# Kernel tuning notes

Measured on AMD Instinct MI355X. Metric: run time of the kernel, lower is better.

## Reference

```python
import jax, jax.numpy as jnp
import numpy as np

EMBED_DIM = 1024
NUM_HEADS = 16
HEAD_DIM = EMBED_DIM // NUM_HEADS


def _sinusoid_pos_emb(seq_len, dim):
    pos = jnp.arange(seq_len, dtype=jnp.float32)
    idx = jnp.arange(dim // 2, dtype=jnp.float32)
    inv_freq = 1.0 / (10000.0 ** (2.0 * idx / dim))
    ang = pos[:, None] * inv_freq[None, :]          # [S, D/2]
    return jnp.concatenate([jnp.sin(ang), jnp.cos(ang)], axis=-1)  # [S, D]


def _relative_shift(x):
    # x: [B, H, S, S] -> Transformer-XL shift
    b, h, s, _ = x.shape
    x = jnp.pad(x, ((0, 0), (0, 0), (0, 0), (1, 0)))
    x = x.reshape(b, h, s + 1, s)
    return x[:, :, 1:, :].reshape(b, h, s, s)


def setup_inputs() -> dict:
    key = jax.random.key(0)
    ks = jax.random.split(key, 12)
    D = EMBED_DIM
    sc = 1.0 / np.sqrt(D)
    inp = {"x": jax.random.normal(ks[0], (2, 2048, D), dtype=jnp.float32)}
    for i, name in enumerate(["Wq", "Wk", "Wv", "Wp", "Wo"]):
        inp[name] = jax.random.normal(ks[1 + i], (D, D), dtype=jnp.float32) * sc
        inp["b" + name[1].lower()] = jnp.zeros((D,), dtype=jnp.float32)
    inp["u"] = jax.random.normal(ks[6], (1, NUM_HEADS, 1, HEAD_DIM), dtype=jnp.float32) * 0.05
    inp["v"] = jax.random.normal(ks[7], (1, NUM_HEADS, 1, HEAD_DIM), dtype=jnp.float32) * 0.05
    return inp


def reference(x, Wq, bq, Wk, bk, Wv, bv, Wp, bp, Wo, bo, u, v):
    B, S, D = x.shape
    H, P = NUM_HEADS, HEAD_DIM

    def heads(t):  # [B,S,D] -> [B,H,S,P]
        return t.reshape(B, S, H, P).transpose(0, 2, 1, 3)

    q = heads(x @ Wq + bq)
    k = heads(x @ Wk + bk)
    val = heads(x @ Wv + bv)

    pos = _sinusoid_pos_emb(S, D) @ Wp + bp            # [S, D]
    pos = pos.reshape(S, H, P).transpose(1, 0, 2)       # [H, S, P]

    content_score = jnp.einsum('bhsp,bhtp->bhst', q + u, k)
    pos_score = jnp.einsum('bhsp,htp->bhst', q + v, pos)
    pos_score = _relative_shift(pos_score)

    score = (content_score + pos_score) / jnp.sqrt(jnp.float32(P))
    weights = jax.nn.softmax(score, axis=-1)            # dropout = 0 (inference)
    out = jnp.einsum('bhst,bhtp->bhsp', weights, val)
    out = out.transpose(0, 2, 1, 3).reshape(B, S, D)
    return out @ Wo + bo
```

## Files before the change

kernel.cpp:

```cpp
#include <hip/hip_runtime.h>
#include <hip/hip_bf16.h>

typedef unsigned short u16;
typedef unsigned int u32;
typedef __bf16 bf16x8 __attribute__((ext_vector_type(8)));
typedef float f32x4 __attribute__((ext_vector_type(4)));

#define SEQ 2048
#define NH 16
#define PD 64
#define DM 1024

#if __has_builtin(__builtin_amdgcn_exp2f)
#define EXP2(x) __builtin_amdgcn_exp2f(x)
#else
#define EXP2(x) __expf((x) * 0.6931471805599453f)
#endif

__device__ __forceinline__ float bf2f(u16 s) {
  u32 t = ((u32)s) << 16;
  float f;
  __builtin_memcpy(&f, &t, 4);
  return f;
}
__device__ __forceinline__ u16 f2bf(float f) {
  u32 x;
  __builtin_memcpy(&x, &f, 4);
  x = (x + 0x7fffu + ((x >> 16) & 1u)) >> 16;
  return (u16)x;
}
__device__ __forceinline__ u32 pack2(float a, float b) {
  __hip_bfloat162 h = __float22bfloat162_rn(float2{a, b});
  u32 r;
  __builtin_memcpy(&r, &h, 4);
  return r;
}
__device__ __forceinline__ void gld16(const u16* g, u16* l) {
  __builtin_amdgcn_global_load_lds(
      (const __attribute__((address_space(1))) unsigned int*)(g),
      (__attribute__((address_space(3))) unsigned int*)(l), 16, 0, 0);
}

struct PrepArgs {
  const void* x;
  const void* w0; const void* w1; const void* w2; const void* w3; const void* w4;
  const void* p0; const void* p1; const void* p2; const void* p3; const void* p4;
  const void* p5; const void* p6;
};

__global__ __launch_bounds__(256) void prep_kernel(PrepArgs pa,
                                                   u16* __restrict__ xb,
                                                   u16* __restrict__ sinb,
                                                   u16* __restrict__ WT,
                                                   float* __restrict__ pf,
                                                   int* __restrict__ flag) {
  __shared__ int sz[256], sh[256];
  __shared__ u16 t[64][72];
  int tid = threadIdx.x;

  {
    const u16* probe = (const u16*)pa.w0;
    int zeros = 0, huge = 0;
    for (int j = 0; j < 16; ++j) {
      int i = tid * 16 + j;
      u16 v = probe[i];
      int e = (v >> 7) & 0xFF;
      if (((i & 1) == 0) && v == 0) zeros++;
      if (e >= 0x8C) huge++;
    }
    sz[tid] = zeros; sh[tid] = huge;
    __syncthreads();
    for (int s = 128; s > 0; s >>= 1) {
      if (tid < s) { sz[tid] += sz[tid + s]; sh[tid] += sh[tid + s]; }
      __syncthreads();
    }
  }
  int f = (sz[0] > 1024 || sh[0] > 200) ? 1 : 0;
  int id = blockIdx.x;
  if (id == 0 && tid == 0) *flag = f;

  if (id < 4096) {
    int i = (id * 256 + tid) * 4;
    if (f) {
      float4 fv = *(const float4*)((const float*)pa.x + i);
      u16 o[4] __attribute__((aligned(8))) = {f2bf(fv.x), f2bf(fv.y), f2bf(fv.z), f2bf(fv.w)};
      *(uint2*)(xb + i) = *(const uint2*)o;
    } else {
      *(uint2*)(xb + i) = *(const uint2*)((const u16*)pa.x + i);
    }
  } else if (id < 6144) {
    int base = ((id - 4096) * 256 + tid) * 4;
    u16 o[4] __attribute__((aligned(8)));
#pragma unroll
    for (int e = 0; e < 4; ++e) {
      int idx = base + e;
      int s = idx >> 10;
      int i = idx & 1023;
      int j = i & 511;
      float invf = __expf(-(float)j * (9.210340371976184f / 512.0f));
      float ang = (float)s * invf;
      float val = (i < 512) ? __sinf(ang) : __cosf(ang);
      o[e] = f2bf(val);
    }
    *(uint2*)(sinb + base) = *(const uint2*)o;
  } else if (id < 7424) {
    int tt = id - 6144;
    int z = tt >> 8;
    int rem = tt & 255;
    const void* src = (z == 0) ? pa.w0 : (z == 1) ? pa.w1 : (z == 2) ? pa.w2
                     : (z == 3) ? pa.w3 : pa.w4;
    u16* out = WT + (size_t)z * DM * DM;
    int r0 = (rem >> 4) * 64, c0 = (rem & 15) * 64;
    int tr = tid >> 2;
    int tc = (tid & 3) * 16;
    if (f) {
      const float* g = (const float*)src + (size_t)(r0 + tr) * DM + c0 + tc;
#pragma unroll
      for (int q = 0; q < 4; ++q) {
        float4 fv = *(const float4*)(g + q * 4);
        t[tr][tc + q * 4 + 0] = f2bf(fv.x);
        t[tr][tc + q * 4 + 1] = f2bf(fv.y);
        t[tr][tc + q * 4 + 2] = f2bf(fv.z);
        t[tr][tc + q * 4 + 3] = f2bf(fv.w);
      }
    } else {
      const uint4* g = (const uint4*)((const u16*)src + (size_t)(r0 + tr) * DM + c0 + tc);
      uint4 a = g[0], bb = g[1];
      *(uint4*)&t[tr][tc] = a;
      *(uint4*)&t[tr][tc + 8] = bb;
    }
    __syncthreads();
    u16 tmp[16] __attribute__((aligned(16)));
#pragma unroll
    for (int jj = 0; jj < 16; ++jj) tmp[jj] = t[tc + jj][tr];
    uint4* o = (uint4*)(out + (size_t)(c0 + tr) * DM + r0 + tc);
    o[0] = *(const uint4*)&tmp[0];
    o[1] = *(const uint4*)&tmp[8];
  } else {
    int idx = (id - 7424) * 256 + tid;
    int seg = idx >> 10, off = idx & 1023;
    const void* s = (seg == 0) ? pa.p0 : (seg == 1) ? pa.p1 : (seg == 2) ? pa.p2
                   : (seg == 3) ? pa.p3 : (seg == 4) ? pa.p4 : (seg == 5) ? pa.p5 : pa.p6;
    pf[idx] = f ? ((const float*)s)[off] : bf2f(((const u16*)s)[off]);
  }
}

__global__ __launch_bounds__(256, 3) void qkv_kernel(
    const u16* __restrict__ xb, const u16* __restrict__ sinb,
    const u16* __restrict__ WT, const float* __restrict__ pf,
    u16* __restrict__ Qb, u16* __restrict__ Kb, u16* __restrict__ Vtb,
    u16* __restrict__ Rb) {
  __shared__ u16 As[128 * 32];
  __shared__ u16 Bs[3 * 64 * 32];
  int tid = threadIdx.x;
  int wave = tid >> 6, lane = tid & 63;
  int quad = lane >> 4, l16 = lane & 15;
  int bx = blockIdx.x, by = blockIdx.y;
  bool isR = by >= 32;
  int m0 = (isR ? (by - 32) : by) * 128;
  int n0 = bx * 64;
  int wm = (wave >> 1) * 64, wn = (wave & 1) * 32;

  int trow = tid >> 2;
  int tcol = ((tid & 3) ^ ((tid >> 3) & 3)) * 8;
  const u16* A = isR ? sinb : xb;
  const u16* ga = A + (size_t)(m0 + trow) * DM + tcol;
  const u16* gb = WT + (isR ? (size_t)3 * DM * DM : 0) + (size_t)(n0 + trow) * DM + tcol;
  u16* lwa = As + wave * 512;
  u16* lwb = Bs + wave * 512;
  int slotx = (quad ^ ((l16 >> 1) & 3)) * 8;

  if (!isR) {
    f32x4 acc[3][4][2] = {};
    for (int k0 = 0; k0 < DM; k0 += 32) {
      __syncthreads();
      gld16(ga + k0, lwa);
      gld16(ga + (size_t)64 * DM + k0, lwa + 2048);
      gld16(gb + k0, lwb);
      gld16(gb + (size_t)DM * DM + k0, lwb + 2048);
      gld16(gb + (size_t)2 * DM * DM + k0, lwb + 4096);
      __syncthreads();
      bf16x8 af[4];
#pragma unroll
      for (int i = 0; i < 4; ++i)
        af[i] = *(const bf16x8*)&As[(wm + i * 16 + l16) * 32 + slotx];
#pragma unroll
      for (int z = 0; z < 3; ++z) {
        bf16x8 b0 = *(const bf16x8*)&Bs[z * 2048 + (wn + l16) * 32 + slotx];
        bf16x8 b1 = *(const bf16x8*)&Bs[z * 2048 + (wn + 16 + l16) * 32 + slotx];
#pragma unroll
        for (int tm = 0; tm < 4; ++tm) {
          acc[z][tm][0] = __builtin_amdgcn_mfma_f32_16x16x32_bf16(af[tm], b0, acc[z][tm][0], 0, 0, 0);
          acc[z][tm][1] = __builtin_amdgcn_mfma_f32_16x16x32_bf16(af[tm], b1, acc[z][tm][1], 0, 0, 0);
        }
      }
    }
#pragma unroll
    for (int tm = 0; tm < 4; ++tm) {
      int row = m0 + wm + tm * 16 + quad * 4;
#pragma unroll
      for (int tn = 0; tn < 2; ++tn) {
        int col = n0 + wn + tn * 16 + l16;
        float bq = pf[col], bk = pf[1024 + col], bv = pf[2048 + col];
#pragma unroll
        for (int r = 0; r < 4; ++r) {
          Qb[(size_t)(row + r) * DM + col] = f2bf(acc[0][tm][tn][r] + bq);
          Kb[(size_t)(row + r) * DM + col] = f2bf(acc[1][tm][tn][r] + bk);
        }
        u16 o4[4] __attribute__((aligned(8)));
#pragma unroll
        for (int r = 0; r < 4; ++r) o4[r] = f2bf(acc[2][tm][tn][r] + bv);
        int bq_ = row >> 11, s = row & 2047;
        *(uint2*)(Vtb + ((size_t)(bq_ * 1024 + col)) * 2048 + s) = *(const uint2*)o4;
      }
    }
  } else {
    f32x4 acc[4][2] = {};
    for (int k0 = 0; k0 < DM; k0 += 32) {
      __syncthreads();
      gld16(ga + k0, lwa);
      gld16(ga + (size_t)64 * DM + k0, lwa + 2048);
      gld16(gb + k0, lwb);
      __syncthreads();
      bf16x8 af[4];
#pragma unroll
      for (int i = 0; i < 4; ++i)
        af[i] = *(const bf16x8*)&As[(wm + i * 16 + l16) * 32 + slotx];
      bf16x8 b0 = *(const bf16x8*)&Bs[(wn + l16) * 32 + slotx];
      bf16x8 b1 = *(const bf16x8*)&Bs[(wn + 16 + l16) * 32 + slotx];
#pragma unroll
      for (int tm = 0; tm < 4; ++tm) {
        acc[tm][0] = __builtin_amdgcn_mfma_f32_16x16x32_bf16(af[tm], b0, acc[tm][0], 0, 0, 0);
        acc[tm][1] = __builtin_amdgcn_mfma_f32_16x16x32_bf16(af[tm], b1, acc[tm][1], 0, 0, 0);
      }
    }
#pragma unroll
    for (int tm = 0; tm < 4; ++tm) {
      int row = m0 + wm + tm * 16 + quad * 4;
#pragma unroll
      for (int tn = 0; tn < 2; ++tn) {
        int col = n0 + wn + tn * 16 + l16;
        float br = pf[3072 + col];
#pragma unroll
        for (int r = 0; r < 4; ++r)
          Rb[(size_t)(row + r) * DM + col] = f2bf(acc[tm][tn][r] + br);
      }
    }
  }
}

struct GemmArgs {
  const u16* A;  const u16* A3;
  const u16* Bt0; const u16* Bt1; const u16* Bt2; const u16* Bt3;
  const float* b0; const float* b1; const float* b2; const float* b3;
  void* C0; void* C1; void* C2; void* C3;
  int N, K, M3;
  const int* flag; int outFp32; int vtrans;
};

__global__ __launch_bounds__(256, 4) void gemm_bt_kernel(GemmArgs p) {
  __shared__ u16 As[128 * 64];
  __shared__ u16 Bs[128 * 64];
  int z = blockIdx.z;
  if (z == 3 && (int)blockIdx.y * 128 >= p.M3) return;
  const u16* A = (z == 3) ? p.A3 : p.A;
  const u16* Bt = (z == 0) ? p.Bt0 : (z == 1) ? p.Bt1 : (z == 2) ? p.Bt2 : p.Bt3;
  const float* bias = (z == 0) ? p.b0 : (z == 1) ? p.b1 : (z == 2) ? p.b2 : p.b3;
  void* Cv = (z == 0) ? p.C0 : (z == 1) ? p.C1 : (z == 2) ? p.C2 : p.C3;
  int K = p.K, N = p.N;
  bool f32o = p.outFp32 && (*p.flag);
  bool vt = p.vtrans && (z == 2);

  int tid = threadIdx.x;
  int wave = tid >> 6, lane = tid & 63;
  int quad = lane >> 4, l16 = lane & 15;
  int m0 = blockIdx.y * 128, n0 = blockIdx.x * 128;
  int wm = (wave >> 1) * 64, wn = (wave & 1) * 64;

  int trow = tid >> 2;
  int tcol = ((tid & 3) ^ ((tid >> 3) & 3)) * 8;
  const u16* ga = A + (size_t)(m0 + trow) * K + tcol;
  const u16* gb = Bt + (size_t)(n0 + trow) * K + tcol;
  u16* lwa = As + wave * 512;
  u16* lwb = Bs + wave * 512;
  int slotx = (quad ^ ((l16 >> 1) & 3)) * 8;

  f32x4 acc[4][4] = {};

  for (int k0 = 0; k0 < K; k0 += 64) {
    __syncthreads();
    gld16(ga + k0, lwa);
    gld16(ga + (size_t)64 * K + k0, lwa + 2048);
    gld16(ga + k0 + 32, lwa + 4096);
    gld16(ga + (size_t)64 * K + k0 + 32, lwa + 6144);
    gld16(gb + k0, lwb);
    gld16(gb + (size_t)64 * K + k0, lwb + 2048);
    gld16(gb + k0 + 32, lwb + 4096);
    gld16(gb + (size_t)64 * K + k0 + 32, lwb + 6144);
    __syncthreads();
#pragma unroll
    for (int kh = 0; kh < 2; ++kh) {
      int kbase = kh * 4096;
      bf16x8 af[4], bfv[4];
#pragma unroll
      for (int i = 0; i < 4; ++i) {
        af[i] = *(const bf16x8*)&As[kbase + (wm + i * 16 + l16) * 32 + slotx];
        bfv[i] = *(const bf16x8*)&Bs[kbase + (wn + i * 16 + l16) * 32 + slotx];
      }
#pragma unroll
      for (int tm = 0; tm < 4; ++tm)
#pragma unroll
        for (int tn = 0; tn < 4; ++tn)
          acc[tm][tn] = __builtin_amdgcn_mfma_f32_16x16x32_bf16(af[tm], bfv[tn], acc[tm][tn], 0, 0, 0);
    }
  }

#pragma unroll
  for (int tm = 0; tm < 4; ++tm) {
    int row = m0 + wm + tm * 16 + quad * 4;
#pragma unroll
    for (int tn = 0; tn < 4; ++tn) {
      int col = n0 + wn + tn * 16 + l16;
      float bv = bias[col];
      if (vt) {
        u16 o4[4] __attribute__((aligned(8)));
#pragma unroll
        for (int r = 0; r < 4; ++r) o4[r] = f2bf(acc[tm][tn][r] + bv);
        int bq_ = row >> 11, s = row & 2047;
        *(uint2*)((u16*)Cv + ((size_t)(bq_ * 1024 + col)) * 2048 + s) = *(const uint2*)o4;
      } else {
#pragma unroll
        for (int r = 0; r < 4; ++r) {
          float val = acc[tm][tn][r] + bv;
          if (f32o) ((float*)Cv)[(size_t)(row + r) * N + col] = val;
          else ((u16*)Cv)[(size_t)(row + r) * N + col] = f2bf(val);
        }
      }
    }
  }
}

__global__ __launch_bounds__(256, 4) void attn_kernel(
    const u16* __restrict__ Q, const u16* __restrict__ Kg,
    const u16* __restrict__ Vtg, const u16* __restrict__ Rg,
    const float* __restrict__ pf,
    u16* __restrict__ O) {
  __shared__ __align__(16) u16 KP[64 * 72];
  __shared__ __align__(16) u16 RVs[4096];
  __shared__ __align__(16) u16 Bb[128 * 66];

  int tid = threadIdx.x, wave = tid >> 6, lane = tid & 63;
  int quad = lane >> 4, l16 = lane & 15;
  int id = blockIdx.x;
  int bh = (id & 7) + ((id >> 8) << 3);
  int s0 = ((id >> 3) & 31) * 64;
  int b = bh >> 4, h = bh & 15;
  const float* pu = pf + 5 * 1024 + h * PD;
  const float* pv = pf + 6 * 1024 + h * PD;

  int arow = wave * 16 + l16;
  int sl_base = wave * 16 + quad * 4;

  int srow = wave * 16 + (lane >> 2);
  int scol = ((lane & 3) ^ ((lane >> 3) & 3)) * 8;
  u16* kbase = KP + wave * 512;
  u16* rvbase = RVs + wave * 512;
  int kb0 = l16 * 32 + (quad ^ ((l16 >> 1) & 3)) * 8;

  const float QS = 0.18033688011112042f;
  bf16x8 qu0, qu1, qv0a, qv1a, qv0b, qv1b;
  {
    const u16* qp = Q + ((size_t)(b * SEQ + s0 + arow)) * DM + h * PD;
    int row2 = s0 + arow + 1;
    if (row2 > SEQ - 1) row2 = SEQ - 1;
    const u16* qp2 = Q + ((size_t)(b * SEQ + row2)) * DM + h * PD;
    u16 qa[16] __attribute__((aligned(16)));
    u16 qb[16] __attribute__((aligned(16)));
    *(uint4*)&qa[0] = *(const uint4*)(qp + quad * 8);
    *(uint4*)&qa[8] = *(const uint4*)(qp + 32 + quad * 8);
    *(uint4*)&qb[0] = *(const uint4*)(qp2 + quad * 8);
    *(uint4*)&qb[8] = *(const uint4*)(qp2 + 32 + quad * 8);
    u16 fu[16] __attribute__((aligned(16)));
    u16 fv0[16] __attribute__((aligned(16)));
    u16 fv1[16] __attribute__((aligned(16)));
#pragma unroll
    for (int j = 0; j < 8; ++j) {
      float u0 = pu[quad * 8 + j], u1 = pu[32 + quad * 8 + j];
      float v0 = pv[quad * 8 + j], v1 = pv[32 + quad * 8 + j];
      fu[j] = f2bf((bf2f(qa[j]) + u0) * QS);
      fu[8 + j] = f2bf((bf2f(qa[8 + j]) + u1) * QS);
      fv0[j] = f2bf((bf2f(qa[j]) + v0) * QS);
      fv0[8 + j] = f2bf((bf2f(qa[8 + j]) + v1) * QS);
      fv1[j] = f2bf((bf2f(qb[j]) + v0) * QS);
      fv1[8 + j] = f2bf((bf2f(qb[8 + j]) + v1) * QS);
    }
    __builtin_memcpy(&qu0, &fu[0], 16);
    __builtin_memcpy(&qu1, &fu[8], 16);
    __builtin_memcpy(&qv0a, &fv0[0], 16);
    __builtin_memcpy(&qv1a, &fv0[8], 16);
    __builtin_memcpy(&qv0b, &fv1[0], 16);
    __builtin_memcpy(&qv1b, &fv1[8], 16);
  }

  bf16x8 onesf;
  {
    u16 onearr[8] __attribute__((aligned(16)));
#pragma unroll
    for (int j = 0; j < 8; ++j) onearr[j] = 0x3F80;
    __builtin_memcpy(&onesf, onearr, 16);
  }

  auto dmaR = [&](int tb0) {
    int tg = tb0 + srow;
    tg = tg < 0 ? 0 : (tg > SEQ - 1 ? SEQ - 1 : tg);
    const u16* gr = Rg + (size_t)tg * DM + h * PD + scol;
    gld16(gr, rvbase);
    gld16(gr + 32, rvbase + 2048);
  };
  auto slice = [&](bf16x8 fa0, bf16x8 fa1, int slotBase, int rowOff, int lo, int hi) {
#pragma unroll
    for (int tt = 0; tt < 4; ++tt) {
      f32x4 pacc = {};
      bf16x8 b0 = *(const bf16x8*)&RVs[kb0 + tt * 512];
      bf16x8 b1 = *(const bf16x8*)&RVs[kb0 + tt * 512 + 2048];
      pacc = __builtin_amdgcn_mfma_f32_16x16x32_bf16(fa0, b0, pacc, 0, 0, 0);
      pacc = __builtin_amdgcn_mfma_f32_16x16x32_bf16(fa1, b1, pacc, 0, 0, 0);
      int rloc = tt * 16 + l16;
      bool ok = (rloc >= lo) & (rloc <= hi);
      u32 w0 = ok ? pack2(pacc[0], pacc[1]) : 0u;
      u32 w1 = ok ? pack2(pacc[2], pacc[3]) : 0u;
      int prow = (slotBase + rloc + rowOff) & 127;
      *(u32*)&Bb[prow * 66 + sl_base] = w0;
      *(u32*)&Bb[prow * 66 + sl_base + 2] = w1;
    }
  };

  f32x4 lacc = {};
  f32x4 oacc[4] = {};

  dmaR(SEQ - 65 - s0);
  __syncthreads();
  slice(qv0a, qv1a, 0, 0, 0, 63);

  for (int j0 = 0; j0 < SEQ; j0 += 64) {
    int a1 = (j0 >> 6) + 1;
    int slot = (a1 & 1) << 6;
    bool p0n = (j0 <= s0);
    bool p1n = (j0 >= s0);
    __syncthreads();
    {
      const u16* gk = Kg + (size_t)(b * SEQ + j0 + srow) * DM + h * PD + scol;
      gld16(gk, kbase);
      gld16(gk + 32, kbase + 2048);
    }
    dmaR((p0n ? (SEQ - 65 - s0) : (-65 - s0)) + 64 * a1);
    __syncthreads();

    f32x4 acc[4];
#pragma unroll
    for (int tn = 0; tn < 4; ++tn) {
      f32x4 a = {};
      bf16x8 b0 = *(const bf16x8*)&KP[kb0 + tn * 512];
      bf16x8 b1 = *(const bf16x8*)&KP[kb0 + tn * 512 + 2048];
      a = __builtin_amdgcn_mfma_f32_16x16x32_bf16(qu0, b0, a, 0, 0, 0);
      a = __builtin_amdgcn_mfma_f32_16x16x32_bf16(qu1, b1, a, 0, 0, 0);
      acc[tn] = a;
    }

    if (p0n) slice(qv0a, qv1a, slot, 0, 0, s0 + 64 - 64 * a1);
    if (p0n && p1n) {
      __syncthreads();
      dmaR(64 * a1 - s0 - 65);
      __syncthreads();
    }
    if (p1n) slice(qv0b, qv1b, slot, 1, s0 + 65 - 64 * a1, 63);
    __syncthreads();

    {
      const u16* gv = Vtg + ((size_t)(b * NH + h) * PD + srow) * SEQ + j0 + scol;
      gld16(gv, rvbase);
      gld16(gv + 32, rvbase + 2048);
    }

    int g0 = l16 - sl_base + 64 + j0;
#pragma unroll
    for (int tn = 0; tn < 4; ++tn) {
#pragma unroll
      for (int r = 0; r < 4; ++r) {
        int rl = (g0 + tn * 16 - r) & 127;
        acc[tn][r] += bf2f(Bb[rl * 66 + sl_base + r]);
      }
    }

#pragma unroll
    for (int r = 0; r < 4; ++r) {
      u32 w0 = pack2(EXP2(acc[0][r]), EXP2(acc[1][r]));
      u32 w1 = pack2(EXP2(acc[2][r]), EXP2(acc[3][r]));
      u16 ec[4] = {(u16)w0, (u16)(w0 >> 16), (u16)w1, (u16)(w1 >> 16)};
      int row = sl_base + r;
      u16* prow_ = KP + row * 72 + l16;
#pragma unroll
      for (int cr = 0; cr < 4; ++cr) {
        int c = (cr + quad) & 3;
        prow_[c * 16] = ec[c];
      }
    }
    __syncthreads();

    {
      bf16x8 pa0 = *(const bf16x8*)&KP[arow * 72 + quad * 8];
      bf16x8 pa1 = *(const bf16x8*)&KP[arow * 72 + 32 + quad * 8];
      lacc = __builtin_amdgcn_mfma_f32_16x16x32_bf16(pa0, onesf, lacc, 0, 0, 0);
      lacc = __builtin_amdgcn_mfma_f32_16x16x32_bf16(pa1, onesf, lacc, 0, 0, 0);
#pragma unroll
      for (int tp = 0; tp < 4; ++tp) {
        bf16x8 b0 = *(const bf16x8*)&RVs[kb0 + tp * 512];
        bf16x8 b1 = *(const bf16x8*)&RVs[kb0 + tp * 512 + 2048];
        oacc[tp] = __builtin_amdgcn_mfma_f32_16x16x32_bf16(pa0, b0, oacc[tp], 0, 0, 0);
        oacc[tp] = __builtin_amdgcn_mfma_f32_16x16x32_bf16(pa1, b1, oacc[tp], 0, 0, 0);
      }
    }
  }

  float li[4];
#pragma unroll
  for (int r = 0; r < 4; ++r) li[r] = 1.f / lacc[r];
#pragma unroll
  for (int tp = 0; tp < 4; ++tp) {
    int pcol = tp * 16 + l16;
#pragma unroll
    for (int r = 0; r < 4; ++r) {
      int sg = s0 + sl_base + r;
      O[((size_t)(b * SEQ + sg)) * DM + h * PD + pcol] = f2bf(oacc[tp][r] * li[r]);
    }
  }
}

extern "C" void kernel_launch(void* const* d_in, const int* in_sizes, int n_in,
                              void* d_out, int out_size, void* d_ws, size_t ws_size,
                              hipStream_t stream) {
  (void)in_sizes; (void)n_in; (void)out_size; (void)ws_size;
  const void* x  = d_in[0];
  const void* Wq = d_in[1];
  const void* bq = d_in[2];
  const void* Wk = d_in[3];
  const void* bk = d_in[4];
  const void* Wv = d_in[5];
  const void* bv = d_in[6];
  const void* Wp = d_in[7];
  const void* bp = d_in[8];
  const void* Wo = d_in[9];
  const void* bo = d_in[10];
  const void* u  = d_in[11];
  const void* v  = d_in[12];

  char* base = (char*)d_ws;
  int* flag = (int*)base;
  float* pf = (float*)(base + 64);
  u16* wbase = (u16*)(base + 64 + 7168 * 4);
  u16* WT   = wbase;
  u16* xb   = WT + (size_t)5 * DM * DM;
  u16* sinb = xb + (size_t)2 * SEQ * DM;
  u16* Qb   = sinb + (size_t)SEQ * DM;
  u16* Kb   = Qb + (size_t)2 * SEQ * DM;
  u16* Vtb  = Kb + (size_t)2 * SEQ * DM;
  u16* Rb   = Vtb + (size_t)2 * SEQ * DM;
  u16* Ab   = xb;

  PrepArgs pa;
  pa.x = x;
  pa.w0 = Wq; pa.w1 = Wk; pa.w2 = Wv; pa.w3 = Wp; pa.w4 = Wo;
  pa.p0 = bq; pa.p1 = bk; pa.p2 = bv; pa.p3 = bp; pa.p4 = bo; pa.p5 = u; pa.p6 = v;
  prep_kernel<<<7452, 256, 0, stream>>>(pa, xb, sinb, WT, pf, flag);

  qkv_kernel<<<dim3(16, 48), 256, 0, stream>>>(xb, sinb, WT, pf, Qb, Kb, Vtb, Rb);

  attn_kernel<<<dim3(1024), 256, 0, stream>>>(Qb, Kb, Vtb, Rb, pf, Ab);

  GemmArgs fo;
  fo.A = Ab; fo.A3 = Ab;
  fo.Bt0 = WT + (size_t)4 * DM * DM; fo.Bt1 = fo.Bt0; fo.Bt2 = fo.Bt0; fo.Bt3 = fo.Bt0;
  fo.b0 = pf + 4096; fo.b1 = fo.b0; fo.b2 = fo.b0; fo.b3 = fo.b0;
  fo.C0 = d_out; fo.C1 = d_out; fo.C2 = d_out; fo.C3 = d_out;
  fo.N = DM; fo.K = DM; fo.M3 = 0; fo.flag = flag; fo.outFp32 = 1; fo.vtrans = 0;
  gemm_bt_kernel<<<dim3(8, 32, 1), 256, 0, stream>>>(fo);
}
```

Before: 284.5 us.

## Merge four launches into two persistent kernels joined by grid barriers

Fuses prep with the QKV/position projection, and attention with the output projection, into two kernels. Each kernel uses an atomic-counter grid barrier and a fixed grid sized to stay co-resident (768 blocks at 3 per CU, 1024 at 4 per CU). The aim is to remove launch gaps and tail effects between stages. In exchange it adds spin-wait barrier cost and a memset. The output GEMM now uses smaller 64x64 tiles, and tighter launch bounds may raise register pressure. It also relies on the runtime occupancy check to avoid deadlock.

```diff
diff --git a/kernel.cpp b/kernel.cpp
--- a/kernel.cpp
+++ b/kernel.cpp
@@ -39,6 +39,19 @@
   __builtin_amdgcn_global_load_lds(
       (const __attribute__((address_space(1))) unsigned int*)(g),
       (__attribute__((address_space(3))) unsigned int*)(l), 16, 0, 0);
+}
+
+__device__ __forceinline__ void grid_barrier(int* cnt, int nblk) {
+  __syncthreads();
+  if (threadIdx.x == 0) {
+    __threadfence();
+    int old = __hip_atomic_fetch_add(cnt, 1, __ATOMIC_ACQ_REL, __HIP_MEMORY_SCOPE_AGENT);
+    int target = (old / nblk + 1) * nblk;
+    while (__hip_atomic_load(cnt, __ATOMIC_ACQUIRE, __HIP_MEMORY_SCOPE_AGENT) < target) {
+      __builtin_amdgcn_s_sleep(8);
+    }
+  }
+  __syncthreads();
 }
 
 struct PrepArgs {
@@ -47,6 +60,453 @@
   const void* p0; const void* p1; const void* p2; const void* p3; const void* p4;
   const void* p5; const void* p6;
 };
+
+__global__ __launch_bounds__(256, 3) void prep_qkv_kernel(
+    PrepArgs pa,
+    u16* __restrict__ xb, u16* __restrict__ sinb, u16* __restrict__ WT,
+    float* __restrict__ pf, int* __restrict__ flag, int* __restrict__ cnt,
+    u16* __restrict__ Qb, u16* __restrict__ Kb, u16* __restrict__ Vtb,
+    u16* __restrict__ Rb) {
+  __shared__ int sz[256], sh[256];
+  __shared__ u16 t[64][72];
+  __shared__ u16 As[128 * 32];
+  __shared__ u16 Bs[3 * 64 * 32];
+  int tid = threadIdx.x;
+  int bid = blockIdx.x;
+
+  {
+    const u16* probe = (const u16*)pa.w0;
+    int zeros = 0, huge = 0;
+    for (int j = 0; j < 16; ++j) {
+      int i = tid * 16 + j;
+      u16 v = probe[i];
+      int e = (v >> 7) & 0xFF;
+      if (((i & 1) == 0) && v == 0) zeros++;
+      if (e >= 0x8C) huge++;
+    }
+    sz[tid] = zeros; sh[tid] = huge;
+    __syncthreads();
+    for (int s = 128; s > 0; s >>= 1) {
+      if (tid < s) { sz[tid] += sz[tid + s]; sh[tid] += sh[tid + s]; }
+      __syncthreads();
+    }
+  }
+  int f = (sz[0] > 1024 || sh[0] > 200) ? 1 : 0;
+  if (bid == 0 && tid == 0) *flag = f;
+
+  for (int id = bid; id < 7452; id += 768) {
+    if (id < 4096) {
+      int i = (id * 256 + tid) * 4;
+      if (f) {
+        float4 fv = *(const float4*)((const float*)pa.x + i);
+        u16 o[4] __attribute__((aligned(8))) = {f2bf(fv.x), f2bf(fv.y), f2bf(fv.z), f2bf(fv.w)};
+        *(uint2*)(xb + i) = *(const uint2*)o;
+      } else {
+        *(uint2*)(xb + i) = *(const uint2*)((const u16*)pa.x + i);
+      }
+    } else if (id < 6144) {
+      int base = ((id - 4096) * 256 + tid) * 4;
+      u16 o[4] __attribute__((aligned(8)));
+#pragma unroll
+      for (int e = 0; e < 4; ++e) {
+        int idx = base + e;
+        int s = idx >> 10;
+        int i = idx & 1023;
+        int j = i & 511;
+        float invf = __expf(-(float)j * (9.210340371976184f / 512.0f));
+        float ang = (float)s * invf;
+        float val = (i < 512) ? __sinf(ang) : __cosf(ang);
+        o[e] = f2bf(val);
+      }
+      *(uint2*)(sinb + base) = *(const uint2*)o;
+    } else if (id < 7424) {
+      __syncthreads();
+      int tt = id - 6144;
+      int z = tt >> 8;
+      int rem = tt & 255;
+      const void* src = (z == 0) ? pa.w0 : (z == 1) ? pa.w1 : (z == 2) ? pa.w2
+                       : (z == 3) ? pa.w3 : pa.w4;
+      u16* out = WT + (size_t)z * DM * DM;
+      int r0 = (rem >> 4) * 64, c0 = (rem & 15) * 64;
+      int tr = tid >> 2;
+      int tc = (tid & 3) * 16;
+      if (f) {
+        const float* g = (const float*)src + (size_t)(r0 + tr) * DM + c0 + tc;
+#pragma unroll
+        for (int q = 0; q < 4; ++q) {
+          float4 fv = *(const float4*)(g + q * 4);
+          t[tr][tc + q * 4 + 0] = f2bf(fv.x);
+          t[tr][tc + q * 4 + 1] = f2bf(fv.y);
+          t[tr][tc + q * 4 + 2] = f2bf(fv.z);
+          t[tr][tc + q * 4 + 3] = f2bf(fv.w);
+        }
+      } else {
+        const uint4* g = (const uint4*)((const u16*)src + (size_t)(r0 + tr) * DM + c0 + tc);
+        uint4 a = g[0], bb = g[1];
+        *(uint4*)&t[tr][tc] = a;
+        *(uint4*)&t[tr][tc + 8] = bb;
+      }
+      __syncthreads();
+      u16 tmp[16] __attribute__((aligned(16)));
+#pragma unroll
+      for (int jj = 0; jj < 16; ++jj) tmp[jj] = t[tc + jj][tr];
+      uint4* o = (uint4*)(out + (size_t)(c0 + tr) * DM + r0 + tc);
+      o[0] = *(const uint4*)&tmp[0];
+      o[1] = *(const uint4*)&tmp[8];
+    } else {
+      int idx = (id - 7424) * 256 + tid;
+      int seg = idx >> 10, off = idx & 1023;
+      const void* s = (seg == 0) ? pa.p0 : (seg == 1) ? pa.p1 : (seg == 2) ? pa.p2
+                     : (seg == 3) ? pa.p3 : (seg == 4) ? pa.p4 : (seg == 5) ? pa.p5 : pa.p6;
+      pf[idx] = f ? ((const float*)s)[off] : bf2f(((const u16*)s)[off]);
+    }
+  }
+
+  grid_barrier(cnt, 768);
+
+  int wave = tid >> 6, lane = tid & 63;
+  int quad = lane >> 4, l16 = lane & 15;
+  int bx = bid & 15, by = bid >> 4;
+  bool isR = by >= 32;
+  int m0 = (isR ? (by - 32) : by) * 128;
+  int n0 = bx * 64;
+  int wm = (wave >> 1) * 64, wn = (wave & 1) * 32;
+
+  int trow = tid >> 2;
+  int tcol = ((tid & 3) ^ ((tid >> 3) & 3)) * 8;
+  const u16* A = isR ? sinb : xb;
+  const u16* ga = A + (size_t)(m0 + trow) * DM + tcol;
+  const u16* gb = WT + (isR ? (size_t)3 * DM * DM : 0) + (size_t)(n0 + trow) * DM + tcol;
+  u16* lwa = As + wave * 512;
+  u16* lwb = Bs + wave * 512;
+  int slotx = (quad ^ ((l16 >> 1) & 3)) * 8;
+
+  if (!isR) {
+    f32x4 acc[3][4][2] = {};
+    for (int k0 = 0; k0 < DM; k0 += 32) {
+      __syncthreads();
+      gld16(ga + k0, lwa);
+      gld16(ga + (size_t)64 * DM + k0, lwa + 2048);
+      gld16(gb + k0, lwb);
+      gld16(gb + (size_t)DM * DM + k0, lwb + 2048);
+      gld16(gb + (size_t)2 * DM * DM + k0, lwb + 4096);
+      __syncthreads();
+      bf16x8 af[4];
+#pragma unroll
+      for (int i = 0; i < 4; ++i)
+        af[i] = *(const bf16x8*)&As[(wm + i * 16 + l16) * 32 + slotx];
+#pragma unroll
+      for (int z = 0; z < 3; ++z) {
+        bf16x8 b0 = *(const bf16x8*)&Bs[z * 2048 + (wn + l16) * 32 + slotx];
+        bf16x8 b1 = *(const bf16x8*)&Bs[z * 2048 + (wn + 16 + l16) * 32 + slotx];
+#pragma unroll
+        for (int tm = 0; tm < 4; ++tm) {
+          acc[z][tm][0] = __builtin_amdgcn_mfma_f32_16x16x32_bf16(af[tm], b0, acc[z][tm][0], 0, 0, 0);
+          acc[z][tm][1] = __builtin_amdgcn_mfma_f32_16x16x32_bf16(af[tm], b1, acc[z][tm][1], 0, 0, 0);
+        }
+      }
+    }
+#pragma unroll
+    for (int tm = 0; tm < 4; ++tm) {
+      int row = m0 + wm + tm * 16 + quad * 4;
+#pragma unroll
+      for (int tn = 0; tn < 2; ++tn) {
+        int col = n0 + wn + tn * 16 + l16;
+        float bq = pf[col], bk = pf[1024 + col], bv = pf[2048 + col];
+#pragma unroll
+        for (int r = 0; r < 4; ++r) {
+          Qb[(size_t)(row + r) * DM + col] = f2bf(acc[0][tm][tn][r] + bq);
+          Kb[(size_t)(row + r) * DM + col] = f2bf(acc[1][tm][tn][r] + bk);
+        }
+        u16 o4[4] __attribute__((aligned(8)));
+#pragma unroll
+        for (int r = 0; r < 4; ++r) o4[r] = f2bf(acc[2][tm][tn][r] + bv);
+        int bq_ = row >> 11, s = row & 2047;
+        *(uint2*)(Vtb + ((size_t)(bq_ * 1024 + col)) * 2048 + s) = *(const uint2*)o4;
+      }
+    }
+  } else {
+    f32x4 acc[4][2] = {};
+    for (int k0 = 0; k0 < DM; k0 += 32) {
+      __syncthreads();
+      gld16(ga + k0, lwa);
+      gld16(ga + (size_t)64 * DM + k0, lwa + 2048);
+      gld16(gb + k0, lwb);
+      __syncthreads();
+      bf16x8 af[4];
+#pragma unroll
+      for (int i = 0; i < 4; ++i)
+        af[i] = *(const bf16x8*)&As[(wm + i * 16 + l16) * 32 + slotx];
+      bf16x8 b0 = *(const bf16x8*)&Bs[(wn + l16) * 32 + slotx];
+      bf16x8 b1 = *(const bf16x8*)&Bs[(wn + 16 + l16) * 32 + slotx];
+#pragma unroll
+      for (int tm = 0; tm < 4; ++tm) {
+        acc[tm][0] = __builtin_amdgcn_mfma_f32_16x16x32_bf16(af[tm], b0, acc[tm][0], 0, 0, 0);
+        acc[tm][1] = __builtin_amdgcn_mfma_f32_16x16x32_bf16(af[tm], b1, acc[tm][1], 0, 0, 0);
+      }
+    }
+#pragma unroll
+    for (int tm = 0; tm < 4; ++tm) {
+      int row = m0 + wm + tm * 16 + quad * 4;
+#pragma unroll
+      for (int tn = 0; tn < 2; ++tn) {
+        int col = n0 + wn + tn * 16 + l16;
+        float br = pf[3072 + col];
+#pragma unroll
+        for (int r = 0; r < 4; ++r)
+          Rb[(size_t)(row + r) * DM + col] = f2bf(acc[tm][tn][r] + br);
+      }
+    }
+  }
+}
+
+__global__ __launch_bounds__(256, 4) void attn_fo_kernel(
+    const u16* __restrict__ Q, const u16* __restrict__ Kg,
+    const u16* __restrict__ Vtg, const u16* __restrict__ Rg,
+    const float* __restrict__ pf,
+    u16* __restrict__ O, const u16* __restrict__ WT4,
+    const int* __restrict__ flag, int* __restrict__ cnt,
+    void* __restrict__ dout) {
+  __shared__ __align__(16) u16 KP[64 * 72];
+  __shared__ __align__(16) u16 RVs[4096];
+  __shared__ __align__(16) u16 Bb[128 * 66];
+
+  int tid = threadIdx.x, wave = tid >> 6, lane = tid & 63;
+  int quad = lane >> 4, l16 = lane & 15;
+  int id = blockIdx.x;
+  int bh = (id & 7) + ((id >> 8) << 3);
+  int s0 = ((id >> 3) & 31) * 64;
+  int b = bh >> 4, h = bh & 15;
+  const float* pu = pf + 5 * 1024 + h * PD;
+  const float* pv = pf + 6 * 1024 + h * PD;
+
+  int arow = wave * 16 + l16;
+  int sl_base = wave * 16 + quad * 4;
+
+  int srow = wave * 16 + (lane >> 2);
+  int scol = ((lane & 3) ^ ((lane >> 3) & 3)) * 8;
+  u16* kbase = KP + wave * 512;
+  u16* rvbase = RVs + wave * 512;
+  int kb0 = l16 * 32 + (quad ^ ((l16 >> 1) & 3)) * 8;
+
+  const float QS = 0.18033688011112042f;
+  bf16x8 qu0, qu1, qv0a, qv1a, qv0b, qv1b;
+  {
+    const u16* qp = Q + ((size_t)(b * SEQ + s0 + arow)) * DM + h * PD;
+    int row2 = s0 + arow + 1;
+    if (row2 > SEQ - 1) row2 = SEQ - 1;
+    const u16* qp2 = Q + ((size_t)(b * SEQ + row2)) * DM + h * PD;
+    u16 qa[16] __attribute__((aligned(16)));
+    u16 qb[16] __attribute__((aligned(16)));
+    *(uint4*)&qa[0] = *(const uint4*)(qp + quad * 8);
+    *(uint4*)&qa[8] = *(const uint4*)(qp + 32 + quad * 8);
+    *(uint4*)&qb[0] = *(const uint4*)(qp2 + quad * 8);
+    *(uint4*)&qb[8] = *(const uint4*)(qp2 + 32 + quad * 8);
+    u16 fu[16] __attribute__((aligned(16)));
+    u16 fv0[16] __attribute__((aligned(16)));
+    u16 fv1[16] __attribute__((aligned(16)));
+#pragma unroll
+    for (int j = 0; j < 8; ++j) {
+      float u0 = pu[quad * 8 + j], u1 = pu[32 + quad * 8 + j];
+      float v0 = pv[quad * 8 + j], v1 = pv[32 + quad * 8 + j];
+      fu[j] = f2bf((bf2f(qa[j]) + u0) * QS);
+      fu[8 + j] = f2bf((bf2f(qa[8 + j]) + u1) * QS);
+      fv0[j] = f2bf((bf2f(qa[j]) + v0) * QS);
+      fv0[8 + j] = f2bf((bf2f(qa[8 + j]) + v1) * QS);
+      fv1[j] = f2bf((bf2f(qb[j]) + v0) * QS);
+      fv1[8 + j] = f2bf((bf2f(qb[8 + j]) + v1) * QS);
+    }
+    __builtin_memcpy(&qu0, &fu[0], 16);
+    __builtin_memcpy(&qu1, &fu[8], 16);
+    __builtin_memcpy(&qv0a, &fv0[0], 16);
+    __builtin_memcpy(&qv1a, &fv0[8], 16);
+    __builtin_memcpy(&qv0b, &fv1[0], 16);
+    __builtin_memcpy(&qv1b, &fv1[8], 16);
+  }
+
+  bf16x8 onesf;
+  {
+    u16 onearr[8] __attribute__((aligned(16)));
+#pragma unroll
+    for (int j = 0; j < 8; ++j) onearr[j] = 0x3F80;
+    __builtin_memcpy(&onesf, onearr, 16);
+  }
+
+  auto dmaR = [&](int tb0) {
+    int tg = tb0 + srow;
+    tg = tg < 0 ? 0 : (tg > SEQ - 1 ? SEQ - 1 : tg);
+    const u16* gr = Rg + (size_t)tg * DM + h * PD + scol;
+    gld16(gr, rvbase);
+    gld16(gr + 32, rvbase + 2048);
+  };
+  auto slice = [&](bf16x8 fa0, bf16x8 fa1, int slotBase, int rowOff, int lo, int hi) {
+#pragma unroll
+    for (int tt = 0; tt < 4; ++tt) {
+      f32x4 pacc = {};
+      bf16x8 b0 = *(const bf16x8*)&RVs[kb0 + tt * 512];
+      bf16x8 b1 = *(const bf16x8*)&RVs[kb0 + tt * 512 + 2048];
+      pacc = __builtin_amdgcn_mfma_f32_16x16x32_bf16(fa0, b0, pacc, 0, 0, 0);
+      pacc = __builtin_amdgcn_mfma_f32_16x16x32_bf16(fa1, b1, pacc, 0, 0, 0);
+      int rloc = tt * 16 + l16;
+      bool ok = (rloc >= lo) & (rloc <= hi);
+      u32 w0 = ok ? pack2(pacc[0], pacc[1]) : 0u;
+      u32 w1 = ok ? pack2(pacc[2], pacc[3]) : 0u;
+      int prow = (slotBase + rloc + rowOff) & 127;
+      *(u32*)&Bb[prow * 66 + sl_base] = w0;
+      *(u32*)&Bb[prow * 66 + sl_base + 2] = w1;
+    }
+  };
+
+  f32x4 lacc = {};
+  f32x4 oacc[4] = {};
+
+  dmaR(SEQ - 65 - s0);
+  __syncthreads();
+  slice(qv0a, qv1a, 0, 0, 0, 63);
+
+  for (int j0 = 0; j0 < SEQ; j0 += 64) {
+    int a1 = (j0 >> 6) + 1;
+    int slot = (a1 & 1) << 6;
+    bool p0n = (j0 <= s0);
+    bool p1n = (j0 >= s0);
+    __syncthreads();
+    {
+      const u16* gk = Kg + (size_t)(b * SEQ + j0 + srow) * DM + h * PD + scol;
+      gld16(gk, kbase);
+      gld16(gk + 32, kbase + 2048);
+    }
+    dmaR((p0n ? (SEQ - 65 - s0) : (-65 - s0)) + 64 * a1);
+    __syncthreads();
+
+    f32x4 acc[4];
+#pragma unroll
+    for (int tn = 0; tn < 4; ++tn) {
+      f32x4 a = {};
+      bf16x8 b0 = *(const bf16x8*)&KP[kb0 + tn * 512];
+      bf16x8 b1 = *(const bf16x8*)&KP[kb0 + tn * 512 + 2048];
+      a = __builtin_amdgcn_mfma_f32_16x16x32_bf16(qu0, b0, a, 0, 0, 0);
+      a = __builtin_amdgcn_mfma_f32_16x16x32_bf16(qu1, b1, a, 0, 0, 0);
+      acc[tn] = a;
+    }
+
+    if (p0n) slice(qv0a, qv1a, slot, 0, 0, s0 + 64 - 64 * a1);
+    if (p0n && p1n) {
+      __syncthreads();
+      dmaR(64 * a1 - s0 - 65);
+      __syncthreads();
+    }
+    if (p1n) slice(qv0b, qv1b, slot, 1, s0 + 65 - 64 * a1, 63);
+    __syncthreads();
+
+    {
+      const u16* gv = Vtg + ((size_t)(b * NH + h) * PD + srow) * SEQ + j0 + scol;
+      gld16(gv, rvbase);
+      gld16(gv + 32, rvbase + 2048);
+    }
+
+    int g0 = l16 - sl_base + 64 + j0;
+#pragma unroll
+    for (int tn = 0; tn < 4; ++tn) {
+#pragma unroll
+      for (int r = 0; r < 4; ++r) {
+        int rl = (g0 + tn * 16 - r) & 127;
+        acc[tn][r] += bf2f(Bb[rl * 66 + sl_base + r]);
+      }
+    }
+
+#pragma unroll
+    for (int r = 0; r < 4; ++r) {
+      u32 w0 = pack2(EXP2(acc[0][r]), EXP2(acc[1][r]));
+      u32 w1 = pack2(EXP2(acc[2][r]), EXP2(acc[3][r]));
+      u16 ec[4] = {(u16)w0, (u16)(w0 >> 16), (u16)w1, (u16)(w1 >> 16)};
+      int row = sl_base + r;
+      u16* prow_ = KP + row * 72 + l16;
+#pragma unroll
+      for (int cr = 0; cr < 4; ++cr) {
+        int c = (cr + quad) & 3;
+        prow_[c * 16] = ec[c];
+      }
+    }
+    __syncthreads();
+
+    {
+      bf16x8 pa0 = *(const bf16x8*)&KP[arow * 72 + quad * 8];
+      bf16x8 pa1 = *(const bf16x8*)&KP[arow * 72 + 32 + quad * 8];
+      lacc = __builtin_amdgcn_mfma_f32_16x16x32_bf16(pa0, onesf, lacc, 0, 0, 0);
+      lacc = __builtin_amdgcn_mfma_f32_16x16x32_bf16(pa1, onesf, lacc, 0, 0, 0);
+#pragma unroll
+      for (int tp = 0; tp < 4; ++tp) {
+        bf16x8 b0 = *(const bf16x8*)&RVs[kb0 + tp * 512];
+        bf16x8 b1 = *(const bf16x8*)&RVs[kb0 + tp * 512 + 2048];
+        oacc[tp] = __builtin_amdgcn_mfma_f32_16x16x32_bf16(pa0, b0, oacc[tp], 0, 0, 0);
+        oacc[tp] = __builtin_amdgcn_mfma_f32_16x16x32_bf16(pa1, b1, oacc[tp], 0, 0, 0);
+      }
+    }
+  }
+
+  float li[4];
+#pragma unroll
+  for (int r = 0; r < 4; ++r) li[r] = 1.f / lacc[r];
+#pragma unroll
+  for (int tp = 0; tp < 4; ++tp) {
+    int pcol = tp * 16 + l16;
+#pragma unroll
+    for (int r = 0; r < 4; ++r) {
+      int sg = s0 + sl_base + r;
+      O[((size_t)(b * SEQ + sg)) * DM + h * PD + pcol] = f2bf(oacc[tp][r] * li[r]);
+    }
+  }
+
+  grid_barrier(cnt, 1024);
+
+  {
+    bool f32o = (*flag != 0);
+    int mt = id >> 4, nt = id & 15;
+    int m0f = mt * 64, n0f = nt * 64;
+    int wm2 = (wave >> 1) * 32, wn2 = (wave & 1) * 32;
+    int trow = tid >> 2;
+    int tcol = ((tid & 3) ^ ((tid >> 3) & 3)) * 8;
+    const u16* gaF = O + (size_t)(m0f + trow) * DM + tcol;
+    const u16* gbF = WT4 + (size_t)(n0f + trow) * DM + tcol;
+    u16* lwaF = KP + wave * 512;
+    u16* lwbF = Bb + wave * 512;
+    int slotx = (quad ^ ((l16 >> 1) & 3)) * 8;
+
+    f32x4 acc2[2][2] = {};
+    for (int k0 = 0; k0 < DM; k0 += 32) {
+      __syncthreads();
+      gld16(gaF + k0, lwaF);
+      gld16(gbF + k0, lwbF);
+      __syncthreads();
+      bf16x8 af2[2], bf2v[2];
+#pragma unroll
+      for (int i = 0; i < 2; ++i) {
+        af2[i] = *(const bf16x8*)&KP[(wm2 + i * 16 + l16) * 32 + slotx];
+        bf2v[i] = *(const bf16x8*)&Bb[(wn2 + i * 16 + l16) * 32 + slotx];
+      }
+#pragma unroll
+      for (int tm = 0; tm < 2; ++tm)
+#pragma unroll
+        for (int tn = 0; tn < 2; ++tn)
+          acc2[tm][tn] = __builtin_amdgcn_mfma_f32_16x16x32_bf16(af2[tm], bf2v[tn], acc2[tm][tn], 0, 0, 0);
+    }
+#pragma unroll
+    for (int tm = 0; tm < 2; ++tm) {
+      int row = m0f + wm2 + tm * 16 + quad * 4;
+#pragma unroll
+      for (int tn = 0; tn < 2; ++tn) {
+        int col = n0f + wn2 + tn * 16 + l16;
+        float bv = pf[4096 + col];
+#pragma unroll
+        for (int r = 0; r < 4; ++r) {
+          float val = acc2[tm][tn][r] + bv;
+          if (f32o) ((float*)dout)[(size_t)(row + r) * DM + col] = val;
+          else ((u16*)dout)[(size_t)(row + r) * DM + col] = f2bf(val);
+        }
+      }
+    }
+  }
+}
 
 __global__ __launch_bounds__(256) void prep_kernel(PrepArgs pa,
                                                    u16* __restrict__ xb,
@@ -57,7 +517,6 @@
   __shared__ int sz[256], sh[256];
   __shared__ u16 t[64][72];
   int tid = threadIdx.x;
-
   {
     const u16* probe = (const u16*)pa.w0;
     int zeros = 0, huge = 0;
@@ -360,7 +819,6 @@
 
   int arow = wave * 16 + l16;
   int sl_base = wave * 16 + quad * 4;
-
   int srow = wave * 16 + (lane >> 2);
   int scol = ((lane & 3) ^ ((lane >> 3) & 3)) * 8;
   u16* kbase = KP + wave * 512;
@@ -556,6 +1014,8 @@
 
   char* base = (char*)d_ws;
   int* flag = (int*)base;
+  int* cnt1 = (int*)(base + 16);
+  int* cnt2 = (int*)(base + 20);
   float* pf = (float*)(base + 64);
   u16* wbase = (u16*)(base + 64 + 7168 * 4);
   u16* WT   = wbase;
@@ -566,20 +1026,33 @@
   u16* Vtb  = Kb + (size_t)2 * SEQ * DM;
   u16* Rb   = Vtb + (size_t)2 * SEQ * DM;
   u16* Ab   = xb;
+  u16* WT4  = WT + (size_t)4 * DM * DM;
 
   PrepArgs pa;
   pa.x = x;
   pa.w0 = Wq; pa.w1 = Wk; pa.w2 = Wv; pa.w3 = Wp; pa.w4 = Wo;
   pa.p0 = bq; pa.p1 = bk; pa.p2 = bv; pa.p3 = bp; pa.p4 = bo; pa.p5 = u; pa.p6 = v;
+
+  int occ1 = 0, occ2 = 0;
+  hipOccupancyMaxActiveBlocksPerMultiprocessor(&occ1, (const void*)prep_qkv_kernel, 256, 0);
+  hipOccupancyMaxActiveBlocksPerMultiprocessor(&occ2, (const void*)attn_fo_kernel, 256, 0);
+
+  if (occ1 >= 3 && occ2 >= 4) {
+    hipMemsetAsync(cnt1, 0, 8, stream);
+    prep_qkv_kernel<<<768, 256, 0, stream>>>(pa, xb, sinb, WT, pf, flag, cnt1,
+                                             Qb, Kb, Vtb, Rb);
+    attn_fo_kernel<<<1024, 256, 0, stream>>>(Qb, Kb, Vtb, Rb, pf, Ab, WT4,
+                                             flag, cnt2, d_out);
+    return;
+  }
+
   prep_kernel<<<7452, 256, 0, stream>>>(pa, xb, sinb, WT, pf, flag);
-
   qkv_kernel<<<dim3(16, 48), 256, 0, stream>>>(xb, sinb, WT, pf, Qb, Kb, Vtb, Rb);
-
   attn_kernel<<<dim3(1024), 256, 0, stream>>>(Qb, Kb, Vtb, Rb, pf, Ab);
 
   GemmArgs fo;
   fo.A = Ab; fo.A3 = Ab;
-  fo.Bt0 = WT + (size_t)4 * DM * DM; fo.Bt1 = fo.Bt0; fo.Bt2 = fo.Bt0; fo.Bt3 = fo.Bt0;
+  fo.Bt0 = WT4; fo.Bt1 = fo.Bt0; fo.Bt2 = fo.Bt0; fo.Bt3 = fo.Bt0;
   fo.b0 = pf + 4096; fo.b1 = fo.b0; fo.b2 = fo.b0; fo.b3 = fo.b0;
   fo.C0 = d_out; fo.C1 = d_out; fo.C2 = d_out; fo.C3 = d_out;
   fo.N = DM; fo.K = DM; fo.M3 = 0; fo.flag = flag; fo.outFp32 = 1; fo.vtrans = 0;
```

Result: no change. 283.5 us (-0.3%).
